# Performance work log

Measured on AMD Instinct MI355X. Metric: run time of the kernel, lower is better.

## Reference

```python
import jax, jax.numpy as jnp
import numpy as np

B, D, H = 128, 256, 512  # batch, input_size, hidden_size; 2 hidden layers
ORDER = 'A'
EPS = 1e-12


def _masks():
    # Standard MADE sequential degrees: inputs 1..D (reversed for order 'B'),
    # hidden degrees cycle over 1..D-1. Hidden mask: >=, output mask: > (strict).
    din = np.arange(1, D + 1) if ORDER == 'A' else np.arange(D, 0, -1)
    dh = (np.arange(H) % (D - 1)) + 1
    m0 = (dh[:, None] >= din[None, :]).astype(np.float32)  # [H, D]
    m1 = (dh[:, None] >= dh[None, :]).astype(np.float32)   # [H, H]
    mo = (din[:, None] > dh[None, :]).astype(np.float32)   # [D, H]
    return jnp.asarray(m0), jnp.asarray(m1), jnp.asarray(mo)


def _made(y, W0, b0, W1, b1, Wo, bo, masks):
    m0, m1, mo = masks
    h = jax.nn.elu(y @ (W0 * m0).T + b0)   # [B, H]
    h = jax.nn.elu(h @ (W1 * m1).T + b1)   # [B, H]
    return h @ (Wo * mo).T + bo            # [B, D]


def setup_inputs() -> dict:
    key = jax.random.key(0)
    ks = jax.random.split(key, 13)
    s_in, s_h = 1.0 / np.sqrt(D), 1.0 / np.sqrt(H)

    def p(k, shape, s):
        return (jax.random.normal(k, shape, jnp.float32) * s).astype(jnp.float32)

    return {
        'x': jax.random.normal(ks[0], (B, D), jnp.float32),
        'mu_W0': p(ks[1], (H, D), s_in), 'mu_b0': jnp.zeros((H,), jnp.float32),
        'mu_W1': p(ks[2], (H, H), s_h),  'mu_b1': jnp.zeros((H,), jnp.float32),
        'mu_Wo': p(ks[3], (D, H), s_h),  'mu_bo': jnp.zeros((D,), jnp.float32),
        'lv_W0': p(ks[4], (H, D), s_in), 'lv_b0': jnp.zeros((H,), jnp.float32),
        'lv_W1': p(ks[5], (H, H), s_h),  'lv_b1': jnp.zeros((H,), jnp.float32),
        'lv_Wo': p(ks[6], (D, H), s_h),  'lv_bo': jnp.zeros((D,), jnp.float32),
    }


def reference(x, mu_W0, mu_b0, mu_W1, mu_b1, mu_Wo, mu_bo,
              lv_W0, lv_b0, lv_W1, lv_b1, lv_Wo, lv_bo):
    masks = _masks()
    idx = jnp.arange(D) if ORDER == 'A' else jnp.arange(D - 1, -1, -1)

    def step(carry, i):
        y, _ = carry
        mu = _made(y, mu_W0, mu_b0, mu_W1, mu_b1, mu_Wo, mu_bo, masks)
        logstd = 0.5 * _made(y, lv_W0, lv_b0, lv_W1, lv_b1, lv_Wo, lv_bo, masks)
        new_col = (x[:, i] - mu[:, i]) / (jnp.exp(logstd[:, i]) + EPS)
        y = y.at[:, i].set(new_col)
        return (y, logstd), None

    init = (jnp.zeros_like(x), jnp.zeros_like(x))
    (y, logstd), _ = jax.lax.scan(step, init, idx)
    return y, logstd.sum(axis=1)
```

## Files before the change

### kernel.cpp

```cpp
#include <hip/hip_runtime.h>

#define DD 256
#define HH 512
#define BB 128
#define TS 4096

#define WAITVM(N) asm volatile("s_waitcnt vmcnt(" #N ")" ::: "memory")
#define SYNC() do { __builtin_amdgcn_s_barrier(); __builtin_amdgcn_sched_barrier(0); } while (0)

__device__ __forceinline__ float elu_f(float x) {
    return x > 0.f ? x : (__expf(x) - 1.f);
}
__device__ __forceinline__ float rlf(float v, int l) {
    return __uint_as_float(__builtin_amdgcn_readlane(__float_as_uint(v), (unsigned)l));
}
__device__ __forceinline__ float f4c(const float4& v, int r) {
    return r == 0 ? v.x : r == 1 ? v.y : r == 2 ? v.z : v.w;
}

__device__ __forceinline__ int pmap(int h) {
    if (h == 510) return 255;
    if (h == 511) return 511;
    return (h < 255) ? (4 * (h & 63) + (h >> 6))
                     : (256 + 4 * ((h - 255) & 63) + ((h - 255) >> 6));
}
__device__ __forceinline__ int p4map(int j) {
    return 4 * (j & 63) + (j >> 6);
}
__device__ __forceinline__ int w1base(int hp) {
    return (hp <= 254) ? hp * TS
         : (hp <= 509) ? (hp - 255) * TS + 1024
         : 255 * TS + ((hp == 510) ? 0 : 1024);
}
__device__ __forceinline__ int wobase(int hp) {
    return (hp <= 254) ? hp * TS + 3072
         : (hp <= 509) ? (hp - 255) * TS + 3584
         : 255 * TS + ((hp == 510) ? 2048 : 2560);
}

__global__ __launch_bounds__(256) void prep(
    const float* __restrict__ w0m_, const float* __restrict__ w0l_,
    const float* __restrict__ w1m_, const float* __restrict__ w1l_,
    const float* __restrict__ wom_, const float* __restrict__ wol_,
    float* __restrict__ tape)
{
    __shared__ float tm[32][33], tl[32][33];
    const int tx = threadIdx.x & 31, ty = threadIdx.x >> 5;
    const unsigned b = blockIdx.x;

    if (b < 256) {
        const int h0 = (int)(b >> 4) << 5, hp0 = (int)(b & 15) << 5;
        #pragma unroll
        for (int j = 0; j < 4; ++j) {
            int r = ty + 8 * j;
            tm[r][tx] = w1m_[(h0 + r) * HH + hp0 + tx];
            tl[r][tx] = w1l_[(h0 + r) * HH + hp0 + tx];
        }
        __syncthreads();
        #pragma unroll
        for (int j = 0; j < 4; ++j) {
            int hp = hp0 + ty + 8 * j;
            int h  = h0 + tx;
            int dh_h = (h <= 254) ? h + 1 : (h <= 509 ? h - 254 : h - 509);
            int dh_p = (hp <= 254) ? hp + 1 : (hp <= 509 ? hp - 254 : hp - 509);
            float mask = (dh_h >= dh_p) ? 1.f : 0.f;
            int base = w1base(hp), p = pmap(h);
            tape[base + p]       = mask * tm[tx][ty + 8 * j];
            tape[base + 512 + p] = mask * tl[tx][ty + 8 * j];
        }
    } else if (b < 384) {
        const int b2 = (int)b - 256;
        const int h0 = (b2 >> 3) << 5, i0 = (b2 & 7) << 5;
        #pragma unroll
        for (int j = 0; j < 4; ++j) {
            int r = ty + 8 * j;
            tm[r][tx] = w0m_[(h0 + r) * DD + i0 + tx];
            tl[r][tx] = w0l_[(h0 + r) * DD + i0 + tx];
        }
        __syncthreads();
        #pragma unroll
        for (int j = 0; j < 4; ++j) {
            int i = i0 + ty + 8 * j;
            int h = h0 + tx;
            int p = pmap(h);
            tape[i * TS + 2048 + p] = tm[tx][ty + 8 * j];
            tape[i * TS + 2560 + p] = tl[tx][ty + 8 * j];
        }
    } else {
        const int b3 = (int)b - 384;
        const int j0 = (b3 >> 4) << 5, hp0 = (b3 & 15) << 5;
        #pragma unroll
        for (int j = 0; j < 4; ++j) {
            int r = ty + 8 * j;
            tm[r][tx] = wom_[(j0 + r) * HH + hp0 + tx];
            tl[r][tx] = wol_[(j0 + r) * HH + hp0 + tx];
        }
        __syncthreads();
        #pragma unroll
        for (int j = 0; j < 4; ++j) {
            int hp = hp0 + ty + 8 * j;
            int jj = j0 + tx;
            int base = wobase(hp), p = p4map(jj);
            tape[base + p]       = tm[tx][ty + 8 * j];
            tape[base + 256 + p] = tl[tx][ty + 8 * j];
        }
    }
}

struct WSet { float4 w[16]; };

__device__ __forceinline__ void stage16(const float* g, float* l, int lane) {
    #pragma unroll
    for (int k = 0; k < 16; ++k) {
        __builtin_amdgcn_global_load_lds(
            (const __attribute__((address_space(1))) void*)(g + 256 * k + 4 * lane),
            (__attribute__((address_space(3))) void*)(l + 256 * k),
            16, 0, 0);
    }
}

__device__ __forceinline__ void rd_set(WSet& S, const float* b, int lane) {
    const float4* p = (const float4*)b;
    #pragma unroll
    for (int k = 0; k < 16; ++k) S.w[k] = p[64 * k + lane];
}

template<int Q, int EX>
__device__ __forceinline__ void stepC(
    int t, int lane, const WSet& S,
    float (&a0m)[8], float (&a0l)[8], float (&a1m)[8], float (&a1l)[8],
    float (&Rm)[4], float (&Rl)[4], float (&yv)[4],
    const float (&xv)[4], const float (&bmv)[4], const float (&blv)[4],
    float& ls_sum,
    const float4& exmA, const float4& exmB, const float4& exlA, const float4& exlB,
    const float4& exwm, const float4& exwl)
{
    float mu = rlf(Rm[Q], t) + rlf(bmv[Q], t);
    float ls = 0.5f * (rlf(Rl[Q], t) + rlf(blv[Q], t));
    ls_sum += ls;
    float v = __fdividef(rlf(xv[Q], t) - mu, __expf(ls) + 1e-12f);
    yv[Q] = (lane == t) ? v : yv[Q];

    #pragma unroll
    for (int r = Q; r < 4; ++r) {
        a0m[r]     += v * f4c(S.w[8], r);
        a0m[4 + r] += v * f4c(S.w[9], r);
        a0l[r]     += v * f4c(S.w[10], r);
        a0l[4 + r] += v * f4c(S.w[11], r);
    }

    float p0m = elu_f(rlf(a0m[Q], t)),     p0l = elu_f(rlf(a0l[Q], t));
    float p1m = elu_f(rlf(a0m[4 + Q], t)), p1l = elu_f(rlf(a0l[4 + Q], t));
    float p2m = 0.f, p2l = 0.f;
    if (EX) {
        p2m = elu_f(rlf(a0m[EX == 1 ? 3 : 7], 63));
        p2l = elu_f(rlf(a0l[EX == 1 ? 3 : 7], 63));
    }

    #pragma unroll
    for (int r = Q; r < 4; ++r) {
        a1m[r]     += f4c(S.w[0], r) * p0m + f4c(S.w[4], r) * p1m;
        a1m[4 + r] += f4c(S.w[1], r) * p0m + f4c(S.w[5], r) * p1m;
        a1l[r]     += f4c(S.w[2], r) * p0l + f4c(S.w[6], r) * p1l;
        a1l[4 + r] += f4c(S.w[3], r) * p0l + f4c(S.w[7], r) * p1l;
    }
    if (EX) {
        #pragma unroll
        for (int r = 0; r < 4; ++r) {
            a1m[r]     += f4c(exmA, r) * p2m;
            a1m[4 + r] += f4c(exmB, r) * p2m;
            a1l[r]     += f4c(exlA, r) * p2l;
            a1l[4 + r] += f4c(exlB, r) * p2l;
        }
    }

    float q0m = elu_f(rlf(a1m[Q], t)),     q0l = elu_f(rlf(a1l[Q], t));
    float q1m = elu_f(rlf(a1m[4 + Q], t)), q1l = elu_f(rlf(a1l[4 + Q], t));
    float q2m = 0.f, q2l = 0.f;
    if (EX) {
        q2m = elu_f(rlf(a1m[EX == 1 ? 3 : 7], 63));
        q2l = elu_f(rlf(a1l[EX == 1 ? 3 : 7], 63));
    }

    #pragma unroll
    for (int r = Q; r < 4; ++r) {
        Rm[r] += f4c(S.w[12], r) * q0m + f4c(S.w[14], r) * q1m;
        Rl[r] += f4c(S.w[13], r) * q0l + f4c(S.w[15], r) * q1l;
    }
    if (EX) {
        #pragma unroll
        for (int r = 0; r < 4; ++r) {
            Rm[r] += f4c(exwm, r) * q2m;
            Rl[r] += f4c(exwl, r) * q2l;
        }
    }
}

__global__ __launch_bounds__(128, 1) void made_main(
    const float* __restrict__ x,
    const float* __restrict__ mu_b0, const float* __restrict__ mu_b1,
    const float* __restrict__ mu_bo,
    const float* __restrict__ lv_b0, const float* __restrict__ lv_b1,
    const float* __restrict__ lv_bo,
    const float* __restrict__ tape,
    float* __restrict__ out)
{
    __shared__ __align__(16) float buf[4][TS];
    const int row = blockIdx.x;

    if (threadIdx.x >= 64) {
        const int lane = threadIdx.x - 64;
        #pragma unroll
        for (int g = 0; g < 3; ++g)
            stage16(tape + (size_t)g * TS, &buf[g][0], lane);
        #pragma unroll 1
        for (int t = 0; t < 255; ++t) {
            WAITVM(32);
            __builtin_amdgcn_s_barrier();
            __builtin_amdgcn_sched_barrier(0);
            int g = t + 3;
            if (g < 255)
                stage16(tape + (size_t)g * TS, &buf[g & 3][0], lane);
        }
        return;
    }

    const int lane = threadIdx.x;

    float a0m[8], a0l[8], a1m[8], a1l[8], Rm[4], Rl[4], yv[4];
    float xv[4], bmv[4], blv[4];
    #pragma unroll
    for (int r = 0; r < 4; ++r) {
        a0m[r]     = mu_b0[lane + 64 * r];
        a0m[4 + r] = mu_b0[255 + lane + 64 * r];
        a0l[r]     = lv_b0[lane + 64 * r];
        a0l[4 + r] = lv_b0[255 + lane + 64 * r];
        a1m[r]     = mu_b1[lane + 64 * r];
        a1m[4 + r] = mu_b1[255 + lane + 64 * r];
        a1l[r]     = lv_b1[lane + 64 * r];
        a1l[4 + r] = lv_b1[255 + lane + 64 * r];
        Rm[r] = 0.f; Rl[r] = 0.f; yv[r] = 0.f;
        xv[r]  = x[row * DD + 64 * r + lane];
        bmv[r] = mu_bo[64 * r + lane];
        blv[r] = lv_bo[64 * r + lane];
    }
    if (lane == 63) {
        a0m[3] = mu_b0[510]; a0m[7] = mu_b0[511];
        a0l[3] = lv_b0[510]; a0l[7] = lv_b0[511];
        a1m[3] = mu_b1[510]; a1m[7] = mu_b1[511];
        a1l[3] = lv_b1[510]; a1l[7] = lv_b1[511];
    }

    const float4* a4 = (const float4*)(tape + 255 * TS);
    float4 e510mA = a4[lane],       e510mB = a4[64 + lane];
    float4 e510lA = a4[128 + lane], e510lB = a4[192 + lane];
    float4 e511mA = a4[256 + lane], e511mB = a4[320 + lane];
    float4 e511lA = a4[384 + lane], e511lB = a4[448 + lane];
    float4 wo510m = a4[512 + lane], wo510l = a4[576 + lane];
    float4 wo511m = a4[640 + lane], wo511l = a4[704 + lane];

    const float4 d4 = make_float4(0.f, 0.f, 0.f, 0.f);

    float ls_sum = 0.f;

    SYNC();
    {
        WSet S; rd_set(S, &buf[0][0], lane);
        stepC<0, 1>(0, lane, S, a0m, a0l, a1m, a1l, Rm, Rl, yv, xv, bmv, blv,
                    ls_sum, e510mA, e510mB, e510lA, e510lB, wo510m, wo510l);
    }

    SYNC();
    {
        WSet S; rd_set(S, &buf[1][0], lane);
        stepC<0, 2>(1, lane, S, a0m, a0l, a1m, a1l, Rm, Rl, yv, xv, bmv, blv,
                    ls_sum, e511mA, e511mB, e511lA, e511lB, wo511m, wo511l);
    }

#define STEP_BODY(Q, t, tl)                                                   \
    {                                                                         \
        SYNC();                                                               \
        WSet S; rd_set(S, &buf[(t) & 3][0], lane);                            \
        stepC<Q, 0>((tl), lane, S, a0m, a0l, a1m, a1l, Rm, Rl, yv,            \
                    xv, bmv, blv, ls_sum, d4, d4, d4, d4, d4, d4);            \
    }

    #pragma unroll 1
    for (int t = 2; t < 64; ++t)    STEP_BODY(0, t, t)
    #pragma unroll 1
    for (int t = 64; t < 128; ++t)  STEP_BODY(1, t, t - 64)
    #pragma unroll 1
    for (int t = 128; t < 192; ++t) STEP_BODY(2, t, t - 128)
    #pragma unroll 1
    for (int t = 192; t < 255; ++t) STEP_BODY(3, t, t - 192)
#undef STEP_BODY

    {
        float mu = rlf(Rm[3], 63) + rlf(bmv[3], 63);
        float ls = 0.5f * (rlf(Rl[3], 63) + rlf(blv[3], 63));
        ls_sum += ls;
        float v = __fdividef(rlf(xv[3], 63) - mu, __expf(ls) + 1e-12f);
        yv[3] = (lane == 63) ? v : yv[3];
    }

    #pragma unroll
    for (int r = 0; r < 4; ++r) out[row * DD + 64 * r + lane] = yv[r];
    if (lane == 0) out[BB * DD + row] = ls_sum;
}

extern "C" void kernel_launch(void* const* d_in, const int* in_sizes, int n_in,
                              void* d_out, int out_size, void* d_ws, size_t ws_size,
                              hipStream_t stream) {
    const float* x     = (const float*)d_in[0];
    const float* mu_W0 = (const float*)d_in[1];
    const float* mu_b0 = (const float*)d_in[2];
    const float* mu_W1 = (const float*)d_in[3];
    const float* mu_b1 = (const float*)d_in[4];
    const float* mu_Wo = (const float*)d_in[5];
    const float* mu_bo = (const float*)d_in[6];
    const float* lv_W0 = (const float*)d_in[7];
    const float* lv_b0 = (const float*)d_in[8];
    const float* lv_W1 = (const float*)d_in[9];
    const float* lv_b1 = (const float*)d_in[10];
    const float* lv_Wo = (const float*)d_in[11];
    const float* lv_bo = (const float*)d_in[12];

    float* tape = (float*)d_ws;

    prep<<<512, 256, 0, stream>>>(mu_W0, lv_W0, mu_W1, lv_W1, mu_Wo, lv_Wo, tape);
    made_main<<<BB, 128, 0, stream>>>(x, mu_b0, mu_b1, mu_bo,
                                      lv_b0, lv_b1, lv_bo, tape, (float*)d_out);
}
```

Before: 185.2 us.

## Split mu and logstd MADE networks across two compute wavefronts with LDS exchange

The single compute wavefront that evaluated both the mu and log-variance MADE chains is replaced by two wavefronts, one per network, plus the existing loader wave. Each step they swap the scalar residual (x-mu) and the inverse scale through a small double-buffered LDS array, synchronised by block barriers. The aim is to halve the serial per-step dependency chain of FMAs, readlanes and elu, at the cost of an extra LDS round-trip per step. The loader's final waits are also tightened so it participates in the extra trailing barrier.

Result: faster. 161.9 us (-12.6%).

```diff
diff --git a/kernel.cpp b/kernel.cpp
--- a/kernel.cpp
+++ b/kernel.cpp
@@ -6,7 +6,6 @@
 #define TS 4096
 
 #define WAITVM(N) asm volatile("s_waitcnt vmcnt(" #N ")" ::: "memory")
-#define SYNC() do { __builtin_amdgcn_s_barrier(); __builtin_amdgcn_sched_barrier(0); } while (0)
 
 __device__ __forceinline__ float elu_f(float x) {
     return x > 0.f ? x : (__expf(x) - 1.f);
@@ -107,8 +106,6 @@
     }
 }
 
-struct WSet { float4 w[16]; };
-
 __device__ __forceinline__ void stage16(const float* g, float* l, int lane) {
     #pragma unroll
     for (int k = 0; k < 16; ++k) {
@@ -119,84 +116,105 @@
     }
 }
 
-__device__ __forceinline__ void rd_set(WSet& S, const float* b, int lane) {
-    const float4* p = (const float4*)b;
-    #pragma unroll
-    for (int k = 0; k < 16; ++k) S.w[k] = p[64 * k + lane];
-}
-
 template<int Q, int EX>
-__device__ __forceinline__ void stepC(
-    int t, int lane, const WSet& S,
-    float (&a0m)[8], float (&a0l)[8], float (&a1m)[8], float (&a1l)[8],
-    float (&Rm)[4], float (&Rl)[4], float (&yv)[4],
-    const float (&xv)[4], const float (&bmv)[4], const float (&blv)[4],
-    float& ls_sum,
-    const float4& exmA, const float4& exmB, const float4& exlA, const float4& exlB,
-    const float4& exwm, const float4& exwl)
+__device__ __forceinline__ void stepM(
+    int tl, int lane, float v, const float4* p,
+    float (&a0m)[8], float (&a1m)[8], float (&Rm)[4], float (&yv)[4],
+    const float4& exA, const float4& exB, const float4& exW)
 {
-    float mu = rlf(Rm[Q], t) + rlf(bmv[Q], t);
-    float ls = 0.5f * (rlf(Rl[Q], t) + rlf(blv[Q], t));
-    ls_sum += ls;
-    float v = __fdividef(rlf(xv[Q], t) - mu, __expf(ls) + 1e-12f);
-    yv[Q] = (lane == t) ? v : yv[Q];
+    float4 w8  = p[64 * 8 + lane],  w9  = p[64 * 9 + lane];
+    float4 w0  = p[64 * 0 + lane],  w4  = p[64 * 4 + lane];
+    float4 w1  = p[64 * 1 + lane],  w5  = p[64 * 5 + lane];
+    float4 w12 = p[64 * 12 + lane], w14 = p[64 * 14 + lane];
+
+    yv[Q] = (lane == tl) ? v : yv[Q];
 
     #pragma unroll
     for (int r = Q; r < 4; ++r) {
-        a0m[r]     += v * f4c(S.w[8], r);
-        a0m[4 + r] += v * f4c(S.w[9], r);
-        a0l[r]     += v * f4c(S.w[10], r);
-        a0l[4 + r] += v * f4c(S.w[11], r);
-    }
-
-    float p0m = elu_f(rlf(a0m[Q], t)),     p0l = elu_f(rlf(a0l[Q], t));
-    float p1m = elu_f(rlf(a0m[4 + Q], t)), p1l = elu_f(rlf(a0l[4 + Q], t));
-    float p2m = 0.f, p2l = 0.f;
+        a0m[r]     += v * f4c(w8, r);
+        a0m[4 + r] += v * f4c(w9, r);
+    }
+    float p0 = elu_f(rlf(a0m[Q], tl));
+    float p1 = elu_f(rlf(a0m[4 + Q], tl));
+    float p2 = 0.f;
+    if (EX) p2 = elu_f(rlf(a0m[EX == 1 ? 3 : 7], 63));
+
+    #pragma unroll
+    for (int r = Q; r < 4; ++r) {
+        a1m[r]     += f4c(w0, r) * p0 + f4c(w4, r) * p1;
+        a1m[4 + r] += f4c(w1, r) * p0 + f4c(w5, r) * p1;
+    }
     if (EX) {
-        p2m = elu_f(rlf(a0m[EX == 1 ? 3 : 7], 63));
-        p2l = elu_f(rlf(a0l[EX == 1 ? 3 : 7], 63));
-    }
+        #pragma unroll
+        for (int r = 0; r < 4; ++r) {
+            a1m[r]     += f4c(exA, r) * p2;
+            a1m[4 + r] += f4c(exB, r) * p2;
+        }
+    }
+
+    float q0 = elu_f(rlf(a1m[Q], tl));
+    float q1 = elu_f(rlf(a1m[4 + Q], tl));
+    float q2 = 0.f;
+    if (EX) q2 = elu_f(rlf(a1m[EX == 1 ? 3 : 7], 63));
+
+    #pragma unroll
+    for (int r = Q; r < 4; ++r)
+        Rm[r] += f4c(w12, r) * q0 + f4c(w14, r) * q1;
+    if (EX) {
+        #pragma unroll
+        for (int r = 0; r < 4; ++r) Rm[r] += f4c(exW, r) * q2;
+    }
+}
+
+template<int Q, int EX>
+__device__ __forceinline__ void stepL(
+    int tl, int lane, float v, const float4* p,
+    float (&a0l)[8], float (&a1l)[8], float (&Rl)[4],
+    const float4& exA, const float4& exB, const float4& exW)
+{
+    float4 w10 = p[64 * 10 + lane], w11 = p[64 * 11 + lane];
+    float4 w2  = p[64 * 2 + lane],  w6  = p[64 * 6 + lane];
+    float4 w3  = p[64 * 3 + lane],  w7  = p[64 * 7 + lane];
+    float4 w13 = p[64 * 13 + lane], w15 = p[64 * 15 + lane];
 
     #pragma unroll
     for (int r = Q; r < 4; ++r) {
-        a1m[r]     += f4c(S.w[0], r) * p0m + f4c(S.w[4], r) * p1m;
-        a1m[4 + r] += f4c(S.w[1], r) * p0m + f4c(S.w[5], r) * p1m;
-        a1l[r]     += f4c(S.w[2], r) * p0l + f4c(S.w[6], r) * p1l;
-        a1l[4 + r] += f4c(S.w[3], r) * p0l + f4c(S.w[7], r) * p1l;
+        a0l[r]     += v * f4c(w10, r);
+        a0l[4 + r] += v * f4c(w11, r);
+    }
+    float p0 = elu_f(rlf(a0l[Q], tl));
+    float p1 = elu_f(rlf(a0l[4 + Q], tl));
+    float p2 = 0.f;
+    if (EX) p2 = elu_f(rlf(a0l[EX == 1 ? 3 : 7], 63));
+
+    #pragma unroll
+    for (int r = Q; r < 4; ++r) {
+        a1l[r]     += f4c(w2, r) * p0 + f4c(w6, r) * p1;
+        a1l[4 + r] += f4c(w3, r) * p0 + f4c(w7, r) * p1;
     }
     if (EX) {
         #pragma unroll
         for (int r = 0; r < 4; ++r) {
-            a1m[r]     += f4c(exmA, r) * p2m;
-            a1m[4 + r] += f4c(exmB, r) * p2m;
-            a1l[r]     += f4c(exlA, r) * p2l;
-            a1l[4 + r] += f4c(exlB, r) * p2l;
-        }
-    }
-
-    float q0m = elu_f(rlf(a1m[Q], t)),     q0l = elu_f(rlf(a1l[Q], t));
-    float q1m = elu_f(rlf(a1m[4 + Q], t)), q1l = elu_f(rlf(a1l[4 + Q], t));
-    float q2m = 0.f, q2l = 0.f;
+            a1l[r]     += f4c(exA, r) * p2;
+            a1l[4 + r] += f4c(exB, r) * p2;
+        }
+    }
+
+    float q0 = elu_f(rlf(a1l[Q], tl));
+    float q1 = elu_f(rlf(a1l[4 + Q], tl));
+    float q2 = 0.f;
+    if (EX) q2 = elu_f(rlf(a1l[EX == 1 ? 3 : 7], 63));
+
+    #pragma unroll
+    for (int r = Q; r < 4; ++r)
+        Rl[r] += f4c(w13, r) * q0 + f4c(w15, r) * q1;
     if (EX) {
-        q2m = elu_f(rlf(a1m[EX == 1 ? 3 : 7], 63));
-        q2l = elu_f(rlf(a1l[EX == 1 ? 3 : 7], 63));
-    }
-
-    #pragma unroll
-    for (int r = Q; r < 4; ++r) {
-        Rm[r] += f4c(S.w[12], r) * q0m + f4c(S.w[14], r) * q1m;
-        Rl[r] += f4c(S.w[13], r) * q0l + f4c(S.w[15], r) * q1l;
-    }
-    if (EX) {
-        #pragma unroll
-        for (int r = 0; r < 4; ++r) {
-            Rm[r] += f4c(exwm, r) * q2m;
-            Rl[r] += f4c(exwl, r) * q2l;
-        }
-    }
-}
-
-__global__ __launch_bounds__(128, 1) void made_main(
+        #pragma unroll
+        for (int r = 0; r < 4; ++r) Rl[r] += f4c(exW, r) * q2;
+    }
+}
+
+__global__ __launch_bounds__(192, 1) void made_main(
     const float* __restrict__ x,
     const float* __restrict__ mu_b0, const float* __restrict__ mu_b1,
     const float* __restrict__ mu_bo,
@@ -206,106 +224,198 @@
     float* __restrict__ out)
 {
     __shared__ __align__(16) float buf[4][TS];
-    const int row = blockIdx.x;
-
-    if (threadIdx.x >= 64) {
-        const int lane = threadIdx.x - 64;
+    __shared__ float exch[2][2];
+    const int row  = blockIdx.x;
+    const int lane = threadIdx.x & 63;
+    const int wid  = threadIdx.x >> 6;
+
+    const float4 d4 = make_float4(0.f, 0.f, 0.f, 0.f);
+
+    if (wid == 2) {
         #pragma unroll
         for (int g = 0; g < 3; ++g)
             stage16(tape + (size_t)g * TS, &buf[g][0], lane);
         #pragma unroll 1
         for (int t = 0; t < 255; ++t) {
-            WAITVM(32);
+            if (t < 253)       { WAITVM(32); }
+            else if (t == 253) { WAITVM(16); }
+            else               { WAITVM(0);  }
             __builtin_amdgcn_s_barrier();
             __builtin_amdgcn_sched_barrier(0);
             int g = t + 3;
             if (g < 255)
                 stage16(tape + (size_t)g * TS, &buf[g & 3][0], lane);
         }
+        __builtin_amdgcn_s_barrier();
         return;
     }
 
-    const int lane = threadIdx.x;
-
-    float a0m[8], a0l[8], a1m[8], a1l[8], Rm[4], Rl[4], yv[4];
-    float xv[4], bmv[4], blv[4];
-    #pragma unroll
-    for (int r = 0; r < 4; ++r) {
-        a0m[r]     = mu_b0[lane + 64 * r];
-        a0m[4 + r] = mu_b0[255 + lane + 64 * r];
-        a0l[r]     = lv_b0[lane + 64 * r];
-        a0l[4 + r] = lv_b0[255 + lane + 64 * r];
-        a1m[r]     = mu_b1[lane + 64 * r];
-        a1m[4 + r] = mu_b1[255 + lane + 64 * r];
-        a1l[r]     = lv_b1[lane + 64 * r];
-        a1l[4 + r] = lv_b1[255 + lane + 64 * r];
-        Rm[r] = 0.f; Rl[r] = 0.f; yv[r] = 0.f;
-        xv[r]  = x[row * DD + 64 * r + lane];
-        bmv[r] = mu_bo[64 * r + lane];
-        blv[r] = lv_bo[64 * r + lane];
-    }
-    if (lane == 63) {
-        a0m[3] = mu_b0[510]; a0m[7] = mu_b0[511];
-        a0l[3] = lv_b0[510]; a0l[7] = lv_b0[511];
-        a1m[3] = mu_b1[510]; a1m[7] = mu_b1[511];
-        a1l[3] = lv_b1[510]; a1l[7] = lv_b1[511];
-    }
-
     const float4* a4 = (const float4*)(tape + 255 * TS);
-    float4 e510mA = a4[lane],       e510mB = a4[64 + lane];
-    float4 e510lA = a4[128 + lane], e510lB = a4[192 + lane];
-    float4 e511mA = a4[256 + lane], e511mB = a4[320 + lane];
-    float4 e511lA = a4[384 + lane], e511lB = a4[448 + lane];
-    float4 wo510m = a4[512 + lane], wo510l = a4[576 + lane];
-    float4 wo511m = a4[640 + lane], wo511l = a4[704 + lane];
-
-    const float4 d4 = make_float4(0.f, 0.f, 0.f, 0.f);
-
-    float ls_sum = 0.f;
-
-    SYNC();
-    {
-        WSet S; rd_set(S, &buf[0][0], lane);
-        stepC<0, 1>(0, lane, S, a0m, a0l, a1m, a1l, Rm, Rl, yv, xv, bmv, blv,
-                    ls_sum, e510mA, e510mB, e510lA, e510lB, wo510m, wo510l);
-    }
-
-    SYNC();
-    {
-        WSet S; rd_set(S, &buf[1][0], lane);
-        stepC<0, 2>(1, lane, S, a0m, a0l, a1m, a1l, Rm, Rl, yv, xv, bmv, blv,
-                    ls_sum, e511mA, e511mB, e511lA, e511lB, wo511m, wo511l);
-    }
-
-#define STEP_BODY(Q, t, tl)                                                   \
+
+    if (wid == 0) {
+        float a0m[8], a1m[8], Rm[4], yv[4], xv[4], bmv[4];
+        #pragma unroll
+        for (int r = 0; r < 4; ++r) {
+            a0m[r]     = mu_b0[lane + 64 * r];
+            a0m[4 + r] = mu_b0[255 + lane + 64 * r];
+            a1m[r]     = mu_b1[lane + 64 * r];
+            a1m[4 + r] = mu_b1[255 + lane + 64 * r];
+            Rm[r] = 0.f; yv[r] = 0.f;
+            xv[r]  = x[row * DD + 64 * r + lane];
+            bmv[r] = mu_bo[64 * r + lane];
+        }
+        if (lane == 63) {
+            a0m[3] = mu_b0[510]; a0m[7] = mu_b0[511];
+            a1m[3] = mu_b1[510]; a1m[7] = mu_b1[511];
+        }
+        float4 e510A = a4[lane],       e510B = a4[64 + lane];
+        float4 e511A = a4[256 + lane], e511B = a4[320 + lane];
+        float4 wo510 = a4[512 + lane], wo511 = a4[640 + lane];
+
+        float d;
+        {
+            float mu = rlf(Rm[0], 0) + rlf(bmv[0], 0);
+            d = rlf(xv[0], 0) - mu;
+            if (lane == 0) exch[0][0] = d;
+        }
+
+        __syncthreads();
+        {
+            float s = exch[0][1];
+            float v = d * s;
+            stepM<0, 1>(0, lane, v, (const float4*)&buf[0][0],
+                        a0m, a1m, Rm, yv, e510A, e510B, wo510);
+            float mu = rlf(Rm[0], 1) + rlf(bmv[0], 1);
+            d = rlf(xv[0], 1) - mu;
+            if (lane == 0) exch[1][0] = d;
+        }
+        __syncthreads();
+        {
+            float s = exch[1][1];
+            float v = d * s;
+            stepM<0, 2>(1, lane, v, (const float4*)&buf[1][0],
+                        a0m, a1m, Rm, yv, e511A, e511B, wo511);
+            float mu = rlf(Rm[0], 2) + rlf(bmv[0], 2);
+            d = rlf(xv[0], 2) - mu;
+            if (lane == 0) exch[0][0] = d;
+        }
+
+#define MBODY(Q, tt, Qn, tn)                                                  \
     {                                                                         \
-        SYNC();                                                               \
-        WSet S; rd_set(S, &buf[(t) & 3][0], lane);                            \
-        stepC<Q, 0>((tl), lane, S, a0m, a0l, a1m, a1l, Rm, Rl, yv,            \
-                    xv, bmv, blv, ls_sum, d4, d4, d4, d4, d4, d4);            \
-    }
-
-    #pragma unroll 1
-    for (int t = 2; t < 64; ++t)    STEP_BODY(0, t, t)
-    #pragma unroll 1
-    for (int t = 64; t < 128; ++t)  STEP_BODY(1, t, t - 64)
-    #pragma unroll 1
-    for (int t = 128; t < 192; ++t) STEP_BODY(2, t, t - 128)
-    #pragma unroll 1
-    for (int t = 192; t < 255; ++t) STEP_BODY(3, t, t - 192)
-#undef STEP_BODY
-
-    {
-        float mu = rlf(Rm[3], 63) + rlf(bmv[3], 63);
-        float ls = 0.5f * (rlf(Rl[3], 63) + rlf(blv[3], 63));
-        ls_sum += ls;
-        float v = __fdividef(rlf(xv[3], 63) - mu, __expf(ls) + 1e-12f);
-        yv[3] = (lane == 63) ? v : yv[3];
-    }
-
-    #pragma unroll
-    for (int r = 0; r < 4; ++r) out[row * DD + 64 * r + lane] = yv[r];
-    if (lane == 0) out[BB * DD + row] = ls_sum;
+        __syncthreads();                                                      \
+        float s_ = exch[(tt) & 1][1];                                         \
+        float v_ = d * s_;                                                    \
+        stepM<Q, 0>((tt) - 64 * (Q), lane, v_,                                \
+                    (const float4*)&buf[(tt) & 3][0],                         \
+                    a0m, a1m, Rm, yv, d4, d4, d4);                            \
+        float mu_ = rlf(Rm[Qn], (tn)) + rlf(bmv[Qn], (tn));                   \
+        d = rlf(xv[Qn], (tn)) - mu_;                                          \
+        if (lane == 0) exch[((tt) + 1) & 1][0] = d;                           \
+    }
+        #pragma unroll 1
+        for (int t = 2; t < 63; ++t)    MBODY(0, t, 0, t + 1)
+        MBODY(0, 63, 1, 0)
+        #pragma unroll 1
+        for (int t = 64; t < 127; ++t)  MBODY(1, t, 1, t - 63)
+        MBODY(1, 127, 2, 0)
+        #pragma unroll 1
+        for (int t = 128; t < 191; ++t) MBODY(2, t, 2, t - 127)
+        MBODY(2, 191, 3, 0)
+        #pragma unroll 1
+        for (int t = 192; t < 254; ++t) MBODY(3, t, 3, t - 191)
+        MBODY(3, 254, 3, 63)
+#undef MBODY
+
+        __syncthreads();
+        {
+            float s = exch[1][1];
+            float v = d * s;
+            yv[3] = (lane == 63) ? v : yv[3];
+        }
+        #pragma unroll
+        for (int r = 0; r < 4; ++r) out[row * DD + 64 * r + lane] = yv[r];
+    } else {
+        float a0l[8], a1l[8], Rl[4], xv[4], blv[4];
+        #pragma unroll
+        for (int r = 0; r < 4; ++r) {
+            a0l[r]     = lv_b0[lane + 64 * r];
+            a0l[4 + r] = lv_b0[255 + lane + 64 * r];
+            a1l[r]     = lv_b1[lane + 64 * r];
+            a1l[4 + r] = lv_b1[255 + lane + 64 * r];
+            Rl[r] = 0.f;
+            xv[r]  = x[row * DD + 64 * r + lane];
+            blv[r] = lv_bo[64 * r + lane];
+        }
+        if (lane == 63) {
+            a0l[3] = lv_b0[510]; a0l[7] = lv_b0[511];
+            a1l[3] = lv_b1[510]; a1l[7] = lv_b1[511];
+        }
+        float4 e510A = a4[128 + lane], e510B = a4[192 + lane];
+        float4 e511A = a4[384 + lane], e511B = a4[448 + lane];
+        float4 wo510 = a4[576 + lane], wo511 = a4[704 + lane];
+
+        float ls_sum = 0.f;
+        float s;
+        {
+            float ls = 0.5f * (rlf(Rl[0], 0) + rlf(blv[0], 0));
+            ls_sum += ls;
+            s = __fdividef(1.f, __expf(ls) + 1e-12f);
+            if (lane == 0) exch[0][1] = s;
+        }
+
+        __syncthreads();
+        {
+            float dd = exch[0][0];
+            float v = dd * s;
+            stepL<0, 1>(0, lane, v, (const float4*)&buf[0][0],
+                        a0l, a1l, Rl, e510A, e510B, wo510);
+            float ls = 0.5f * (rlf(Rl[0], 1) + rlf(blv[0], 1));
+            ls_sum += ls;
+            s = __fdividef(1.f, __expf(ls) + 1e-12f);
+            if (lane == 0) exch[1][1] = s;
+        }
+        __syncthreads();
+        {
+            float dd = exch[1][0];
+            float v = dd * s;
+            stepL<0, 2>(1, lane, v, (const float4*)&buf[1][0],
+                        a0l, a1l, Rl, e511A, e511B, wo511);
+            float ls = 0.5f * (rlf(Rl[0], 2) + rlf(blv[0], 2));
+            ls_sum += ls;
+            s = __fdividef(1.f, __expf(ls) + 1e-12f);
+            if (lane == 0) exch[0][1] = s;
+        }
+
+#define LBODY(Q, tt, Qn, tn)                                                  \
+    {                                                                         \
+        __syncthreads();                                                      \
+        float d_ = exch[(tt) & 1][0];                                         \
+        float v_ = d_ * s;                                                    \
+        stepL<Q, 0>((tt) - 64 * (Q), lane, v_,                                \
+                    (const float4*)&buf[(tt) & 3][0],                         \
+                    a0l, a1l, Rl, d4, d4, d4);                                \
+        float ls_ = 0.5f * (rlf(Rl[Qn], (tn)) + rlf(blv[Qn], (tn)));          \
+        ls_sum += ls_;                                                        \
+        s = __fdividef(1.f, __expf(ls_) + 1e-12f);                            \
+        if (lane == 0) exch[((tt) + 1) & 1][1] = s;                           \
+    }
+        #pragma unroll 1
+        for (int t = 2; t < 63; ++t)    LBODY(0, t, 0, t + 1)
+        LBODY(0, 63, 1, 0)
+        #pragma unroll 1
+        for (int t = 64; t < 127; ++t)  LBODY(1, t, 1, t - 63)
+        LBODY(1, 127, 2, 0)
+        #pragma unroll 1
+        for (int t = 128; t < 191; ++t) LBODY(2, t, 2, t - 127)
+        LBODY(2, 191, 3, 0)
+        #pragma unroll 1
+        for (int t = 192; t < 254; ++t) LBODY(3, t, 3, t - 191)
+        LBODY(3, 254, 3, 63)
+#undef LBODY
+
+        __syncthreads();
+        if (lane == 0) out[BB * DD + row] = ls_sum;
+    }
 }
 
 extern "C" void kernel_launch(void* const* d_in, const int* in_sizes, int n_in,
@@ -328,6 +438,6 @@
     float* tape = (float*)d_ws;
 
     prep<<<512, 256, 0, stream>>>(mu_W0, lv_W0, mu_W1, lv_W1, mu_Wo, lv_Wo, tape);
-    made_main<<<BB, 128, 0, stream>>>(x, mu_b0, mu_b1, mu_bo,
+    made_main<<<BB, 192, 0, stream>>>(x, mu_b0, mu_b1, mu_bo,
                                       lv_b0, lv_b1, lv_bo, tape, (float*)d_out);
 }
```

## Prefetch next step's weights from LDS and compute next output column early

Applied to the files above, without the earlier changes.

Software-pipelines the sequential loop. The next step's weight set is read from LDS right after the current step's FMAs and pinned in registers. The next column's mu/logstd transform is now computed vectorised on every lane (one exp and divide per lane) instead of via scalar readlanes at the start of the step, taking it off the serial critical path. The producer wave's vmcnt wait is tightened, and logstd is summed per lane with a final shuffle reduction. This raises register pressure, since two weight sets are live, and the waitcnt change alters how far the LDS prefetch runs ahead.

Result: faster. 178.4 us (-3.7%).

```diff
diff --git a/kernel.cpp b/kernel.cpp
--- a/kernel.cpp
+++ b/kernel.cpp
@@ -6,7 +6,7 @@
 #define TS 4096
 
 #define WAITVM(N) asm volatile("s_waitcnt vmcnt(" #N ")" ::: "memory")
-#define SYNC() do { __builtin_amdgcn_s_barrier(); __builtin_amdgcn_sched_barrier(0); } while (0)
+#define PIN4(v) asm volatile("" :: "v"((v).x), "v"((v).y), "v"((v).z), "v"((v).w))
 
 __device__ __forceinline__ float elu_f(float x) {
     return x > 0.f ? x : (__expf(x) - 1.f);
@@ -107,8 +107,6 @@
     }
 }
 
-struct WSet { float4 w[16]; };
-
 __device__ __forceinline__ void stage16(const float* g, float* l, int lane) {
     #pragma unroll
     for (int k = 0; k < 16; ++k) {
@@ -119,27 +117,33 @@
     }
 }
 
-__device__ __forceinline__ void rd_set(WSet& S, const float* b, int lane) {
+struct WSet { float4 w[16]; };
+
+__device__ __forceinline__ void rdW(WSet& S, const float* b, int lane) {
     const float4* p = (const float4*)b;
-    #pragma unroll
-    for (int k = 0; k < 16; ++k) S.w[k] = p[64 * k + lane];
+    S.w[8]  = p[64 * 8 + lane];  S.w[9]  = p[64 * 9 + lane];
+    S.w[10] = p[64 * 10 + lane]; S.w[11] = p[64 * 11 + lane];
+    S.w[0]  = p[64 * 0 + lane];  S.w[4]  = p[64 * 4 + lane];
+    S.w[1]  = p[64 * 1 + lane];  S.w[5]  = p[64 * 5 + lane];
+    S.w[2]  = p[64 * 2 + lane];  S.w[6]  = p[64 * 6 + lane];
+    S.w[3]  = p[64 * 3 + lane];  S.w[7]  = p[64 * 7 + lane];
+    S.w[12] = p[64 * 12 + lane]; S.w[14] = p[64 * 14 + lane];
+    S.w[13] = p[64 * 13 + lane]; S.w[15] = p[64 * 15 + lane];
+}
+__device__ __forceinline__ void pinW(const WSet& S) {
+    #pragma unroll
+    for (int k = 0; k < 16; ++k) PIN4(S.w[k]);
 }
 
 template<int Q, int EX>
-__device__ __forceinline__ void stepC(
-    int t, int lane, const WSet& S,
+__device__ __forceinline__ void stepF(
+    int tl, int lane, float v, const WSet& S,
     float (&a0m)[8], float (&a0l)[8], float (&a1m)[8], float (&a1l)[8],
     float (&Rm)[4], float (&Rl)[4], float (&yv)[4],
-    const float (&xv)[4], const float (&bmv)[4], const float (&blv)[4],
-    float& ls_sum,
     const float4& exmA, const float4& exmB, const float4& exlA, const float4& exlB,
     const float4& exwm, const float4& exwl)
 {
-    float mu = rlf(Rm[Q], t) + rlf(bmv[Q], t);
-    float ls = 0.5f * (rlf(Rl[Q], t) + rlf(blv[Q], t));
-    ls_sum += ls;
-    float v = __fdividef(rlf(xv[Q], t) - mu, __expf(ls) + 1e-12f);
-    yv[Q] = (lane == t) ? v : yv[Q];
+    yv[Q] = (lane == tl) ? v : yv[Q];
 
     #pragma unroll
     for (int r = Q; r < 4; ++r) {
@@ -149,8 +153,8 @@
         a0l[4 + r] += v * f4c(S.w[11], r);
     }
 
-    float p0m = elu_f(rlf(a0m[Q], t)),     p0l = elu_f(rlf(a0l[Q], t));
-    float p1m = elu_f(rlf(a0m[4 + Q], t)), p1l = elu_f(rlf(a0l[4 + Q], t));
+    float p0m = elu_f(rlf(a0m[Q], tl)),     p0l = elu_f(rlf(a0l[Q], tl));
+    float p1m = elu_f(rlf(a0m[4 + Q], tl)), p1l = elu_f(rlf(a0l[4 + Q], tl));
     float p2m = 0.f, p2l = 0.f;
     if (EX) {
         p2m = elu_f(rlf(a0m[EX == 1 ? 3 : 7], 63));
@@ -174,8 +178,8 @@
         }
     }
 
-    float q0m = elu_f(rlf(a1m[Q], t)),     q0l = elu_f(rlf(a1l[Q], t));
-    float q1m = elu_f(rlf(a1m[4 + Q], t)), q1l = elu_f(rlf(a1l[4 + Q], t));
+    float q0m = elu_f(rlf(a1m[Q], tl)),     q0l = elu_f(rlf(a1l[Q], tl));
+    float q1m = elu_f(rlf(a1m[4 + Q], tl)), q1l = elu_f(rlf(a1l[4 + Q], tl));
     float q2m = 0.f, q2l = 0.f;
     if (EX) {
         q2m = elu_f(rlf(a1m[EX == 1 ? 3 : 7], 63));
@@ -206,16 +210,19 @@
     float* __restrict__ out)
 {
     __shared__ __align__(16) float buf[4][TS];
-    const int row = blockIdx.x;
-
-    if (threadIdx.x >= 64) {
-        const int lane = threadIdx.x - 64;
+    const int row  = blockIdx.x;
+    const int lane = threadIdx.x & 63;
+    const int wid  = threadIdx.x >> 6;
+
+    const float4 d4 = make_float4(0.f, 0.f, 0.f, 0.f);
+
+    if (wid == 1) {
         #pragma unroll
         for (int g = 0; g < 3; ++g)
             stage16(tape + (size_t)g * TS, &buf[g][0], lane);
         #pragma unroll 1
         for (int t = 0; t < 255; ++t) {
-            WAITVM(32);
+            if (t < 253) { WAITVM(16); } else { WAITVM(0); }
             __builtin_amdgcn_s_barrier();
             __builtin_amdgcn_sched_barrier(0);
             int g = t + 3;
@@ -224,8 +231,6 @@
         }
         return;
     }
-
-    const int lane = threadIdx.x;
 
     float a0m[8], a0l[8], a1m[8], a1l[8], Rm[4], Rl[4], yv[4];
     float xv[4], bmv[4], blv[4];
@@ -259,53 +264,85 @@
     float4 wo510m = a4[512 + lane], wo510l = a4[576 + lane];
     float4 wo511m = a4[640 + lane], wo511l = a4[704 + lane];
 
-    const float4 d4 = make_float4(0.f, 0.f, 0.f, 0.f);
-
-    float ls_sum = 0.f;
-
-    SYNC();
+    float ls_part = 0.f;
+    float vloc;
     {
-        WSet S; rd_set(S, &buf[0][0], lane);
-        stepC<0, 1>(0, lane, S, a0m, a0l, a1m, a1l, Rm, Rl, yv, xv, bmv, blv,
-                    ls_sum, e510mA, e510mB, e510lA, e510lB, wo510m, wo510l);
-    }
-
-    SYNC();
+        float d0  = xv[0] - (Rm[0] + bmv[0]);
+        float ls0 = 0.5f * (Rl[0] + blv[0]);
+        float s0  = __fdividef(1.f, __expf(ls0) + 1e-12f);
+        ls_part += (lane == 0) ? ls0 : 0.f;
+        vloc = d0 * s0;
+    }
+
+    WSet W;
+
+    __syncthreads();
+    rdW(W, &buf[0][0], lane);
     {
-        WSet S; rd_set(S, &buf[1][0], lane);
-        stepC<0, 2>(1, lane, S, a0m, a0l, a1m, a1l, Rm, Rl, yv, xv, bmv, blv,
-                    ls_sum, e511mA, e511mB, e511lA, e511lB, wo511m, wo511l);
-    }
-
-#define STEP_BODY(Q, t, tl)                                                   \
+        float v = rlf(vloc, 0);
+        stepF<0, 1>(0, lane, v, W, a0m, a0l, a1m, a1l, Rm, Rl, yv,
+                    e510mA, e510mB, e510lA, e510lB, wo510m, wo510l);
+        rdW(W, &buf[1][0], lane);
+        float d_  = xv[0] - (Rm[0] + bmv[0]);
+        float ls_ = 0.5f * (Rl[0] + blv[0]);
+        float s_  = __fdividef(1.f, __expf(ls_) + 1e-12f);
+        ls_part += (lane == 1) ? ls_ : 0.f;
+        vloc = d_ * s_;
+        pinW(W);
+    }
+
+    __syncthreads();
+    {
+        float v = rlf(vloc, 1);
+        stepF<0, 2>(1, lane, v, W, a0m, a0l, a1m, a1l, Rm, Rl, yv,
+                    e511mA, e511mB, e511lA, e511lB, wo511m, wo511l);
+        rdW(W, &buf[2][0], lane);
+        float d_  = xv[0] - (Rm[0] + bmv[0]);
+        float ls_ = 0.5f * (Rl[0] + blv[0]);
+        float s_  = __fdividef(1.f, __expf(ls_) + 1e-12f);
+        ls_part += (lane == 2) ? ls_ : 0.f;
+        vloc = d_ * s_;
+        pinW(W);
+    }
+
+#define FBODY(Q, tt, Qn, tn, PREF)                                            \
     {                                                                         \
-        SYNC();                                                               \
-        WSet S; rd_set(S, &buf[(t) & 3][0], lane);                            \
-        stepC<Q, 0>((tl), lane, S, a0m, a0l, a1m, a1l, Rm, Rl, yv,            \
-                    xv, bmv, blv, ls_sum, d4, d4, d4, d4, d4, d4);            \
+        __syncthreads();                                                      \
+        float v_ = rlf(vloc, (tt) & 63);                                      \
+        stepF<Q, 0>((tt) & 63, lane, v_, W, a0m, a0l, a1m, a1l, Rm, Rl, yv,   \
+                    d4, d4, d4, d4, d4, d4);                                  \
+        if (PREF) rdW(W, &buf[((tt) + 1) & 3][0], lane);                      \
+        float dn_  = xv[Qn] - (Rm[Qn] + bmv[Qn]);                             \
+        float lsn_ = 0.5f * (Rl[Qn] + blv[Qn]);                               \
+        float sn_  = __fdividef(1.f, __expf(lsn_) + 1e-12f);                  \
+        ls_part += (lane == (tn)) ? lsn_ : 0.f;                               \
+        vloc = dn_ * sn_;                                                     \
+        if (PREF) pinW(W);                                                    \
     }
 
     #pragma unroll 1
-    for (int t = 2; t < 64; ++t)    STEP_BODY(0, t, t)
+    for (int t = 2; t < 63; ++t)    FBODY(0, t, 0, t + 1, 1)
+    FBODY(0, 63, 1, 0, 1)
     #pragma unroll 1
-    for (int t = 64; t < 128; ++t)  STEP_BODY(1, t, t - 64)
+    for (int t = 64; t < 127; ++t)  FBODY(1, t, 1, t - 63, 1)
+    FBODY(1, 127, 2, 0, 1)
     #pragma unroll 1
-    for (int t = 128; t < 192; ++t) STEP_BODY(2, t, t - 128)
+    for (int t = 128; t < 191; ++t) FBODY(2, t, 2, t - 127, 1)
+    FBODY(2, 191, 3, 0, 1)
     #pragma unroll 1
-    for (int t = 192; t < 255; ++t) STEP_BODY(3, t, t - 192)
-#undef STEP_BODY
-
-    {
-        float mu = rlf(Rm[3], 63) + rlf(bmv[3], 63);
-        float ls = 0.5f * (rlf(Rl[3], 63) + rlf(blv[3], 63));
-        ls_sum += ls;
-        float v = __fdividef(rlf(xv[3], 63) - mu, __expf(ls) + 1e-12f);
-        yv[3] = (lane == 63) ? v : yv[3];
-    }
+    for (int t = 192; t < 254; ++t) FBODY(3, t, 3, t - 191, 1)
+    FBODY(3, 254, 3, 63, 0)
+#undef FBODY
+
+    yv[3] = (lane == 63) ? vloc : yv[3];
 
     #pragma unroll
     for (int r = 0; r < 4; ++r) out[row * DD + 64 * r + lane] = yv[r];
-    if (lane == 0) out[BB * DD + row] = ls_sum;
+
+    #pragma unroll
+    for (int off = 32; off; off >>= 1)
+        ls_part += __shfl_down(ls_part, off);
+    if (lane == 0) out[BB * DD + row] = ls_part;
 }
 
 extern "C" void kernel_launch(void* const* d_in, const int* in_sizes, int n_in,
```
